# Kernel optimization log

Measured on AMD Instinct MI355X. Metric: run time of the kernel, lower is better.

The kernel has to match this reference:

```python
import jax, jax.numpy as jnp
import numpy as np

NUM_CLASSES = 256
WEIGHT = 0.0005
EPS = 1e-12  # torch F.normalize eps


def setup_inputs() -> dict:
    key = jax.random.key(0)
    k1, k2 = jax.random.split(key)
    features = jax.random.normal(k1, (32768, 1024), dtype=jnp.float32)
    labels = jax.random.randint(k2, (32768,), 0, NUM_CLASSES, dtype=jnp.int32)
    return {"features": features, "labels": labels}


def _centroid_loss(features, labels):
    B, D = features.shape
    # row-wise L2 normalize (torch F.normalize: x / max(||x||, eps))
    norms = jnp.linalg.norm(features, axis=1, keepdims=True)
    f = features / jnp.maximum(norms, EPS)

    ones = jnp.ones((B,), f.dtype)
    counts = jax.ops.segment_sum(ones, labels, num_segments=NUM_CLASSES)  # [C]
    sums = jax.ops.segment_sum(f, labels, num_segments=NUM_CLASSES)       # [C, D]

    # rank of each sample within its class (order of first appearance),
    # matching the row order of features[class_mask] in the original loop
    onehot = jax.nn.one_hot(labels, NUM_CLASSES, dtype=jnp.int32)          # [B, C]
    rank = jnp.take_along_axis(jnp.cumsum(onehot, axis=0), labels[:, None].astype(jnp.int32), axis=1)[:, 0] - 1

    # idx_table[c, r] = global index of the r-th member of class c; sentinel B if none
    idx_table = jnp.full((NUM_CLASSES, B), B, dtype=jnp.int32)
    idx_table = idx_table.at[labels, rank].set(jnp.arange(B, dtype=jnp.int32))

    # NOTE: the original code indexes class_features with the GLOBAL index i
    # (arange(n_c) != i), i.e. it excludes the member of the class at position i,
    # and excludes nothing when i >= n_c. We reproduce that exactly.
    arange_b = jnp.arange(B)
    k = idx_table[labels, arange_b]            # class member at in-class position i (global i)
    valid_excl = k < B                          # exclusion only happens when i < class size
    excl_feat = jnp.where(valid_excl[:, None], f[jnp.where(valid_excl, k, 0)], 0.0)

    n_c = counts[labels]                        # class size per sample (float)
    denom = jnp.where(valid_excl, n_c - 1.0, n_c)
    denom = jnp.maximum(denom, 1.0)             # safe for masked-out singleton classes
    centroid = (sums[labels] - excl_feat) / denom[:, None]

    dist = jnp.mean((f - centroid) ** 2, axis=1)  # F.mse_loss(..., reduction='mean')
    contrib = jnp.where(n_c > 1.0, dist, 0.0)     # skip classes with <=1 sample
    return WEIGHT * jnp.sum(contrib) / B


def reference(features, labels):
    return _centroid_loss(features, labels)
```

## Files before the change

kernel.cpp:

```cpp
#include <hip/hip_runtime.h>

#define BN 32768
#define DN 1024
#define CN 256
#define RCAP 512

__device__ __forceinline__ float dot4(float4 a, float4 b) {
    return a.x*b.x + a.y*b.y + a.z*b.z + a.w*b.w;
}

__global__ void __launch_bounds__(1024) k_main(const float4* __restrict__ x4,
                                               const int* __restrict__ labels,
                                               int* __restrict__ idx,
                                               int* __restrict__ counts,
                                               float* __restrict__ rnorm,
                                               float* __restrict__ sums,
                                               float* __restrict__ snorm2,
                                               float* __restrict__ acc) {
    __shared__ unsigned int packed[BN / 4];
    __shared__ int sic[RCAP];
    __shared__ int wcnt[16];
    __shared__ float facc[(DN / 4) * 5];
    __shared__ float wred[4];

    const int c = blockIdx.x;
    const int t = threadIdx.x;

    for (int w = t; w < BN / 4; w += 1024) {
        const int4 v = ((const int4*)labels)[w];
        packed[w] = (unsigned int)(v.x & 255)
                  | ((unsigned int)(v.y & 255) << 8)
                  | ((unsigned int)(v.z & 255) << 16)
                  | ((unsigned int)(v.w & 255) << 24);
    }
    for (int i = t; i < (DN / 4) * 5; i += 1024) facc[i] = 0.0f;
    __syncthreads();

    const int wave = t >> 6, lane = t & 63;
    const unsigned long long lt = (lane == 0) ? 0ull : (~0ull >> (64 - lane));
    const int ch0 = wave * 32, ch1 = ch0 + 32;

    int cnt = 0;
    for (int ch = ch0; ch < ch1; ++ch) {
        const int gi = ch * 64 + lane;
        const int lab = (packed[gi >> 2] >> ((gi & 3) * 8)) & 255;
        cnt += __popcll(__ballot(lab == c));
    }
    if (lane == 0) wcnt[wave] = cnt;
    __syncthreads();

    int base = 0, ntot = 0;
    for (int w2 = 0; w2 < 16; ++w2) {
        const int v = wcnt[w2];
        if (w2 < wave) base += v;
        ntot += v;
    }

    for (int ch = ch0; ch < ch1; ++ch) {
        const int gi = ch * 64 + lane;
        const int lab = (packed[gi >> 2] >> ((gi & 3) * 8)) & 255;
        const bool pred = (lab == c);
        const unsigned long long mask = __ballot(pred);
        if (pred) {
            const int pos = base + __popcll(mask & lt);
            if (pos < RCAP) { sic[pos] = gi; idx[c * RCAP + pos] = gi; }
        }
        base += __popcll(mask);
    }
    if (t == 0) counts[c] = ntot;
    __syncthreads();

    const int nn = min(ntot, RCAP);
    float4 a0 = make_float4(0.f, 0.f, 0.f, 0.f), a1 = a0, a2 = a0, a3 = a0;
    for (int r = wave; r < nn; r += 16) {
        const int row = sic[r];
        const float4* b4 = x4 + (size_t)row * 256;
        const float4 v0 = b4[lane];
        const float4 v1 = b4[lane + 64];
        const float4 v2 = b4[lane + 128];
        const float4 v3 = b4[lane + 192];
        float ss = dot4(v0, v0) + dot4(v1, v1) + dot4(v2, v2) + dot4(v3, v3);
#pragma unroll
        for (int off = 32; off; off >>= 1) ss += __shfl_xor(ss, off, 64);
        const float rn = 1.0f / fmaxf(sqrtf(ss), 1e-12f);
        if (lane == 0) rnorm[row] = rn;
        a0.x += v0.x * rn; a0.y += v0.y * rn; a0.z += v0.z * rn; a0.w += v0.w * rn;
        a1.x += v1.x * rn; a1.y += v1.y * rn; a1.z += v1.z * rn; a1.w += v1.w * rn;
        a2.x += v2.x * rn; a2.y += v2.y * rn; a2.z += v2.z * rn; a2.w += v2.w * rn;
        a3.x += v3.x * rn; a3.y += v3.y * rn; a3.z += v3.z * rn; a3.w += v3.w * rn;
    }

    {
        const int q0 = lane, q1 = lane + 64, q2 = lane + 128, q3 = lane + 192;
        atomicAdd(&facc[5 * q0 + 0], a0.x); atomicAdd(&facc[5 * q0 + 1], a0.y);
        atomicAdd(&facc[5 * q0 + 2], a0.z); atomicAdd(&facc[5 * q0 + 3], a0.w);
        atomicAdd(&facc[5 * q1 + 0], a1.x); atomicAdd(&facc[5 * q1 + 1], a1.y);
        atomicAdd(&facc[5 * q1 + 2], a1.z); atomicAdd(&facc[5 * q1 + 3], a1.w);
        atomicAdd(&facc[5 * q2 + 0], a2.x); atomicAdd(&facc[5 * q2 + 1], a2.y);
        atomicAdd(&facc[5 * q2 + 2], a2.z); atomicAdd(&facc[5 * q2 + 3], a2.w);
        atomicAdd(&facc[5 * q3 + 0], a3.x); atomicAdd(&facc[5 * q3 + 1], a3.y);
        atomicAdd(&facc[5 * q3 + 2], a3.z); atomicAdd(&facc[5 * q3 + 3], a3.w);
    }
    __syncthreads();

    float d = 0.0f;
    if (t < 256) {
        float4 tot;
        tot.x = facc[5 * t + 0]; tot.y = facc[5 * t + 1];
        tot.z = facc[5 * t + 2]; tot.w = facc[5 * t + 3];
        ((float4*)sums)[(size_t)c * 256 + t] = tot;
        d = dot4(tot, tot);
    }
    if (wave < 4) {
#pragma unroll
        for (int off = 32; off; off >>= 1) d += __shfl_xor(d, off, 64);
        if (lane == 0) wred[wave] = d;
    }
    __syncthreads();
    if (t == 0) {
        const float s2 = wred[0] + wred[1] + wred[2] + wred[3];
        snorm2[c] = s2;
        if (ntot > 1) {
            const float nf = (float)ntot;
            atomicAdd(acc, (nf - s2 / nf) * (1.0f / DN));
        }
    }
}

__global__ void __launch_bounds__(256) k_corr(const float4* __restrict__ x4,
                                              const int* __restrict__ labels,
                                              const int* __restrict__ counts,
                                              const int* __restrict__ idx,
                                              const float* __restrict__ rnorm,
                                              const float* __restrict__ sums,
                                              const float* __restrict__ snorm2,
                                              float* __restrict__ acc) {
    const int i = blockIdx.x;
    const int c = labels[i];
    const int n = counts[c];
    if (i >= n || n < 2 || i >= RCAP) return;
    const int k = idx[c * RCAP + i];
    const int t = threadIdx.x;

    const float4 xi = x4[(size_t)i * 256 + t];
    const float4 xk = x4[(size_t)k * 256 + t];
    const float4 s  = ((const float4*)sums)[(size_t)c * 256 + t];

    float d0 = dot4(xi, s);
    float d1 = dot4(xi, xk);
    float d2 = dot4(xk, s);
    float d3 = dot4(xk, xk);
#pragma unroll
    for (int off = 32; off; off >>= 1) {
        d0 += __shfl_xor(d0, off, 64);
        d1 += __shfl_xor(d1, off, 64);
        d2 += __shfl_xor(d2, off, 64);
        d3 += __shfl_xor(d3, off, 64);
    }
    __shared__ float4 wred[4];
    if ((t & 63) == 0) wred[t >> 6] = make_float4(d0, d1, d2, d3);
    __syncthreads();
    if (t == 0) {
        const float xiS  = wred[0].x + wred[1].x + wred[2].x + wred[3].x;
        const float xixk = wred[0].y + wred[1].y + wred[2].y + wred[3].y;
        const float xkS  = wred[0].z + wred[1].z + wred[2].z + wred[3].z;
        const float xkxk = wred[0].w + wred[1].w + wred[2].w + wred[3].w;
        const float rni = rnorm[i], rnk = rnorm[k], s2 = snorm2[c];
        const float fiS  = rni * xiS;
        const float fifk = rni * rnk * xixk;
        const float Sfk  = rnk * xkS;
        const float fk2  = rnk * rnk * xkxk;
        const float nf = (float)n;
        const float dd = nf - 1.0f;
        const float naive = -2.0f * fiS / nf + s2 / (nf * nf);
        const float corr  = -2.0f * (fiS - fifk) / dd + (s2 - 2.0f * Sfk + fk2) / (dd * dd);
        atomicAdd(acc, (corr - naive) * (1.0f / DN));
    }
}

__global__ void k_fin(const float* __restrict__ acc, float* __restrict__ out) {
    out[0] = (0.0005f / (float)BN) * acc[0];
}

extern "C" void kernel_launch(void* const* d_in, const int* in_sizes, int n_in,
                              void* d_out, int out_size, void* d_ws, size_t ws_size,
                              hipStream_t stream) {
    const float* features = (const float*)d_in[0];
    const int* labels = (const int*)d_in[1];
    float* out = (float*)d_out;

    char* ws = (char*)d_ws;
    float* rnorm  = (float*)(ws + 0);
    float* sums   = (float*)(ws + 131072);
    int*   idx    = (int*)  (ws + 1179648);
    int*   counts = (int*)  (ws + 1703936);
    float* snorm2 = (float*)(ws + 1704960);
    float* acc    = (float*)(ws + 1705984);

    const float4* x4 = (const float4*)features;

    hipMemsetAsync(acc, 0, sizeof(float), stream);
    k_main<<<CN, 1024, 0, stream>>>(x4, labels, idx, counts, rnorm, sums, snorm2, acc);
    k_corr<<<RCAP, 256, 0, stream>>>(x4, labels, counts, idx, rnorm, sums, snorm2, acc);
    k_fin<<<1, 1, 0, stream>>>(acc, out);
}
```

Baseline: 222.1 us.

## Split per-class kernel into compact, multi-block gather, and reduce stages

The single per-class kernel (256 blocks of 1024 threads) becomes three kernels. A label-compaction kernel builds the index lists, a gather kernel spreads each class over 8 blocks of 256 threads with software prefetch of the next row, and a reduce kernel sums the 8 partial centroid sums. This raises the block count to fill more CUs and hides the latency of the feature gathers. In exchange it adds two launches and an 8 MB partials round-trip through global memory.

```diff
diff --git a/kernel.cpp b/kernel.cpp
--- a/kernel.cpp
+++ b/kernel.cpp
@@ -4,41 +4,33 @@
 #define DN 1024
 #define CN 256
 #define RCAP 512
+#define SUBS 8
+#define WPB 4
 
 __device__ __forceinline__ float dot4(float4 a, float4 b) {
     return a.x*b.x + a.y*b.y + a.z*b.z + a.w*b.w;
 }
 
-__global__ void __launch_bounds__(1024) k_main(const float4* __restrict__ x4,
-                                               const int* __restrict__ labels,
-                                               int* __restrict__ idx,
-                                               int* __restrict__ counts,
-                                               float* __restrict__ rnorm,
-                                               float* __restrict__ sums,
-                                               float* __restrict__ snorm2,
-                                               float* __restrict__ acc) {
+__global__ void __launch_bounds__(256) kc_compact(const int* __restrict__ labels,
+                                                  int* __restrict__ idx,
+                                                  int* __restrict__ counts) {
     __shared__ unsigned int packed[BN / 4];
-    __shared__ int sic[RCAP];
-    __shared__ int wcnt[16];
-    __shared__ float facc[(DN / 4) * 5];
-    __shared__ float wred[4];
-
+    __shared__ int wcnt[4];
     const int c = blockIdx.x;
     const int t = threadIdx.x;
 
-    for (int w = t; w < BN / 4; w += 1024) {
+    for (int w = t; w < BN / 4; w += 256) {
         const int4 v = ((const int4*)labels)[w];
         packed[w] = (unsigned int)(v.x & 255)
                   | ((unsigned int)(v.y & 255) << 8)
                   | ((unsigned int)(v.z & 255) << 16)
                   | ((unsigned int)(v.w & 255) << 24);
     }
-    for (int i = t; i < (DN / 4) * 5; i += 1024) facc[i] = 0.0f;
     __syncthreads();
 
     const int wave = t >> 6, lane = t & 63;
     const unsigned long long lt = (lane == 0) ? 0ull : (~0ull >> (64 - lane));
-    const int ch0 = wave * 32, ch1 = ch0 + 32;
+    const int ch0 = wave * 128, ch1 = ch0 + 128;
 
     int cnt = 0;
     for (int ch = ch0; ch < ch1; ++ch) {
@@ -49,12 +41,8 @@
     if (lane == 0) wcnt[wave] = cnt;
     __syncthreads();
 
-    int base = 0, ntot = 0;
-    for (int w2 = 0; w2 < 16; ++w2) {
-        const int v = wcnt[w2];
-        if (w2 < wave) base += v;
-        ntot += v;
-    }
+    int base = 0;
+    for (int w2 = 0; w2 < wave; ++w2) base += wcnt[w2];
 
     for (int ch = ch0; ch < ch1; ++ch) {
         const int gi = ch * 64 + lane;
@@ -63,33 +51,64 @@
         const unsigned long long mask = __ballot(pred);
         if (pred) {
             const int pos = base + __popcll(mask & lt);
-            if (pos < RCAP) { sic[pos] = gi; idx[c * RCAP + pos] = gi; }
+            if (pos < RCAP) idx[c * RCAP + pos] = gi;
         }
         base += __popcll(mask);
     }
-    if (t == 0) counts[c] = ntot;
-    __syncthreads();
-
-    const int nn = min(ntot, RCAP);
+    if (t == 0) counts[c] = wcnt[0] + wcnt[1] + wcnt[2] + wcnt[3];
+}
+
+__global__ void __launch_bounds__(256, 4) k_gather(const float4* __restrict__ x4,
+                                                   const int* __restrict__ idx,
+                                                   const int* __restrict__ counts,
+                                                   float* __restrict__ rnorm,
+                                                   float4* __restrict__ partials) {
+    __shared__ float facc[(DN / 4) * 5];
+    const int b = blockIdx.x;
+    const int c = b >> 3;
+    const int sub = b & 7;
+    const int t = threadIdx.x;
+    const int wave = t >> 6, lane = t & 63;
+    const int ws = sub * WPB + wave;
+    const int nn = min(counts[c], RCAP);
+
+    for (int i = t; i < (DN / 4) * 5; i += 256) facc[i] = 0.0f;
+
+    int myidx = 0;
+    {
+        const int r = ws + 32 * lane;
+        if (lane < 16 && r < nn) myidx = idx[c * RCAP + r];
+    }
+    const int nrows = (nn > ws) ? ((nn - ws + 31) >> 5) : 0;
+
     float4 a0 = make_float4(0.f, 0.f, 0.f, 0.f), a1 = a0, a2 = a0, a3 = a0;
-    for (int r = wave; r < nn; r += 16) {
-        const int row = sic[r];
-        const float4* b4 = x4 + (size_t)row * 256;
-        const float4 v0 = b4[lane];
-        const float4 v1 = b4[lane + 64];
-        const float4 v2 = b4[lane + 128];
-        const float4 v3 = b4[lane + 192];
-        float ss = dot4(v0, v0) + dot4(v1, v1) + dot4(v2, v2) + dot4(v3, v3);
-#pragma unroll
-        for (int off = 32; off; off >>= 1) ss += __shfl_xor(ss, off, 64);
-        const float rn = 1.0f / fmaxf(sqrtf(ss), 1e-12f);
-        if (lane == 0) rnorm[row] = rn;
-        a0.x += v0.x * rn; a0.y += v0.y * rn; a0.z += v0.z * rn; a0.w += v0.w * rn;
-        a1.x += v1.x * rn; a1.y += v1.y * rn; a1.z += v1.z * rn; a1.w += v1.w * rn;
-        a2.x += v2.x * rn; a2.y += v2.y * rn; a2.z += v2.z * rn; a2.w += v2.w * rn;
-        a3.x += v3.x * rn; a3.y += v3.y * rn; a3.z += v3.z * rn; a3.w += v3.w * rn;
-    }
-
+
+    if (nrows > 0) {
+        int row = __shfl(myidx, 0, 64);
+        const float4* rb = x4 + (size_t)row * 256;
+        float4 v0 = rb[lane], v1 = rb[lane + 64], v2 = rb[lane + 128], v3 = rb[lane + 192];
+        for (int j = 0; j < nrows; ++j) {
+            int nrow = 0;
+            float4 n0 = make_float4(0.f, 0.f, 0.f, 0.f), n1 = n0, n2 = n0, n3 = n0;
+            if (j + 1 < nrows) {
+                nrow = __shfl(myidx, j + 1, 64);
+                const float4* nb = x4 + (size_t)nrow * 256;
+                n0 = nb[lane]; n1 = nb[lane + 64]; n2 = nb[lane + 128]; n3 = nb[lane + 192];
+            }
+            float ss = dot4(v0, v0) + dot4(v1, v1) + dot4(v2, v2) + dot4(v3, v3);
+#pragma unroll
+            for (int off = 32; off; off >>= 1) ss += __shfl_xor(ss, off, 64);
+            const float rn = 1.0f / fmaxf(sqrtf(ss), 1e-12f);
+            if (lane == 0) rnorm[row] = rn;
+            a0.x += v0.x * rn; a0.y += v0.y * rn; a0.z += v0.z * rn; a0.w += v0.w * rn;
+            a1.x += v1.x * rn; a1.y += v1.y * rn; a1.z += v1.z * rn; a1.w += v1.w * rn;
+            a2.x += v2.x * rn; a2.y += v2.y * rn; a2.z += v2.z * rn; a2.w += v2.w * rn;
+            a3.x += v3.x * rn; a3.y += v3.y * rn; a3.z += v3.z * rn; a3.w += v3.w * rn;
+            row = nrow; v0 = n0; v1 = n1; v2 = n2; v3 = n3;
+        }
+    }
+
+    __syncthreads();
     {
         const int q0 = lane, q1 = lane + 64, q2 = lane + 128, q3 = lane + 192;
         atomicAdd(&facc[5 * q0 + 0], a0.x); atomicAdd(&facc[5 * q0 + 1], a0.y);
@@ -103,25 +122,40 @@
     }
     __syncthreads();
 
-    float d = 0.0f;
-    if (t < 256) {
-        float4 tot;
-        tot.x = facc[5 * t + 0]; tot.y = facc[5 * t + 1];
-        tot.z = facc[5 * t + 2]; tot.w = facc[5 * t + 3];
-        ((float4*)sums)[(size_t)c * 256 + t] = tot;
-        d = dot4(tot, tot);
-    }
-    if (wave < 4) {
-#pragma unroll
-        for (int off = 32; off; off >>= 1) d += __shfl_xor(d, off, 64);
-        if (lane == 0) wred[wave] = d;
-    }
+    const float4 tot = make_float4(facc[5 * t + 0], facc[5 * t + 1],
+                                   facc[5 * t + 2], facc[5 * t + 3]);
+    partials[(size_t)b * 256 + t] = tot;
+}
+
+__global__ void __launch_bounds__(256) k_red(const float4* __restrict__ partials,
+                                             const int* __restrict__ counts,
+                                             float* __restrict__ sums,
+                                             float* __restrict__ snorm2,
+                                             float* __restrict__ acc) {
+    __shared__ float wred[4];
+    const int c = blockIdx.x;
+    const int t = threadIdx.x;
+    const int wave = t >> 6, lane = t & 63;
+
+    float4 tot = make_float4(0.f, 0.f, 0.f, 0.f);
+#pragma unroll
+    for (int s = 0; s < SUBS; ++s) {
+        const float4 p = partials[(size_t)(c * SUBS + s) * 256 + t];
+        tot.x += p.x; tot.y += p.y; tot.z += p.z; tot.w += p.w;
+    }
+    ((float4*)sums)[(size_t)c * 256 + t] = tot;
+
+    float d = dot4(tot, tot);
+#pragma unroll
+    for (int off = 32; off; off >>= 1) d += __shfl_xor(d, off, 64);
+    if (lane == 0) wred[wave] = d;
     __syncthreads();
     if (t == 0) {
         const float s2 = wred[0] + wred[1] + wred[2] + wred[3];
         snorm2[c] = s2;
-        if (ntot > 1) {
-            const float nf = (float)ntot;
+        const int n = counts[c];
+        if (n > 1) {
+            const float nf = (float)n;
             atomicAdd(acc, (nf - s2 / nf) * (1.0f / DN));
         }
     }
@@ -190,17 +224,20 @@
     float* out = (float*)d_out;
 
     char* ws = (char*)d_ws;
-    float* rnorm  = (float*)(ws + 0);
-    float* sums   = (float*)(ws + 131072);
-    int*   idx    = (int*)  (ws + 1179648);
-    int*   counts = (int*)  (ws + 1703936);
-    float* snorm2 = (float*)(ws + 1704960);
-    float* acc    = (float*)(ws + 1705984);
+    float4* partials = (float4*)(ws + 0);
+    float*  rnorm    = (float*)(ws + 8388608);
+    float*  sums     = (float*)(ws + 8519680);
+    int*    idx      = (int*)  (ws + 9568256);
+    int*    counts   = (int*)  (ws + 10092544);
+    float*  snorm2   = (float*)(ws + 10093568);
+    float*  acc      = (float*)(ws + 10094592);
 
     const float4* x4 = (const float4*)features;
 
     hipMemsetAsync(acc, 0, sizeof(float), stream);
-    k_main<<<CN, 1024, 0, stream>>>(x4, labels, idx, counts, rnorm, sums, snorm2, acc);
+    kc_compact<<<CN, 256, 0, stream>>>(labels, idx, counts);
+    k_gather<<<CN * SUBS, 256, 0, stream>>>(x4, idx, counts, rnorm, partials);
+    k_red<<<CN, 256, 0, stream>>>(partials, counts, sums, snorm2, acc);
     k_corr<<<RCAP, 256, 0, stream>>>(x4, labels, counts, idx, rnorm, sums, snorm2, acc);
     k_fin<<<1, 1, 0, stream>>>(acc, out);
 }
```

New measurement: 255.4 us. 1.15x slower.
